# Kernel tuning notes

Measured on AMD Instinct MI355X. Metric: run time of the kernel, lower is better.

## Reference

```python
import jax, jax.numpy as jnp
import numpy as np

N = 16384      # batch (samples / graph nodes)
H = 256        # hid_dim
PRED_LEN = 24


def setup_inputs() -> dict:
    key = jax.random.key(0)
    ks = jax.random.split(key, 9)
    s = 1.0 / np.sqrt(H)  # PyTorch default init bound for GRUCell / Linear(H, 1)
    return {
        "encoder_out": jax.random.normal(ks[0], (N, H), dtype=jnp.float32),
        # input_proj = Linear(1, H): weight [H,1] flattened to [H], bound 1/sqrt(1)=1
        "w_proj": jax.random.uniform(ks[1], (H,), jnp.float32, -1.0, 1.0),
        "b_proj": jax.random.uniform(ks[2], (H,), jnp.float32, -1.0, 1.0),
        # GRUCell weights: [3H, H] ordered (reset, update, new) as in PyTorch
        "W_ih": jax.random.uniform(ks[3], (3 * H, H), jnp.float32, -s, s),
        "b_ih": jax.random.uniform(ks[4], (3 * H,), jnp.float32, -s, s),
        "W_hh": jax.random.uniform(ks[5], (3 * H, H), jnp.float32, -s, s),
        "b_hh": jax.random.uniform(ks[6], (3 * H,), jnp.float32, -s, s),
        # output_layer = Linear(H, 1): weight [1,H] flattened to [H]
        "w_out": jax.random.uniform(ks[7], (H,), jnp.float32, -s, s),
        "b_out": jax.random.uniform(ks[8], (1,), jnp.float32, -s, s),
    }


def reference(encoder_out, w_proj, b_proj, W_ih, b_ih, W_hh, b_hh, w_out, b_out):
    def step(carry, _):
        h, x = carry                       # h: [N,H], x: [N,1] scalar step input
        px = x * w_proj + b_proj           # input_proj(Linear(1,H)) -> [N,H]
        gi = px @ W_ih.T + b_ih            # [N,3H]
        gh = h @ W_hh.T + b_hh             # [N,3H]
        i_r, i_z, i_n = jnp.split(gi, 3, axis=1)
        h_r, h_z, h_n = jnp.split(gh, 3, axis=1)
        r = jax.nn.sigmoid(i_r + h_r)
        z = jax.nn.sigmoid(i_z + h_z)
        n = jnp.tanh(i_n + r * h_n)
        h_new = (1.0 - z) * n + z * h      # PyTorch GRUCell update
        pred = (h_new @ w_out)[:, None] + b_out  # output_layer -> [N,1]
        next_x = jax.lax.stop_gradient(pred)     # matches pred_t.detach()
        return (h_new, next_x), pred[:, 0]

    x0 = jnp.zeros((encoder_out.shape[0], 1), dtype=encoder_out.dtype)  # start token
    _, preds = jax.lax.scan(step, (encoder_out, x0), None, length=PRED_LEN)
    return preds.T  # [N, pred_len]
```

## Files before the change

### kernel.cpp

```cpp
#include <hip/hip_runtime.h>
#include <hip/hip_bf16.h>

#define NS 16384
#define H 256
#define TH 768
#define PRED 24
#define LDA 272
#define WS_NEEDED (425984)

typedef short bf16x8 __attribute__((ext_vector_type(8)));
typedef float floatx4 __attribute__((ext_vector_type(4)));

__device__ __forceinline__ float b2f(unsigned short u) {
    return __uint_as_float(((unsigned int)u) << 16);
}
__device__ __forceinline__ unsigned short f2b(float f) {
    unsigned int u = __float_as_uint(f);
    return (unsigned short)((u + 0x7FFFu + ((u >> 16) & 1u)) >> 16);
}
__device__ __forceinline__ float fsig(float v) {
    return __builtin_amdgcn_rcpf(1.0f + __expf(-v));
}
__device__ __forceinline__ float ftanh(float v) {
    return 1.0f - 2.0f * __builtin_amdgcn_rcpf(1.0f + __expf(2.0f * v));
}

__global__ void prep_proj(const void* __restrict__ WihP, const void* __restrict__ wprojP,
                          const void* __restrict__ bprojP, const void* __restrict__ bihP,
                          const void* __restrict__ bhhP, const void* __restrict__ woutP,
                          const void* __restrict__ boutP,
                          float* __restrict__ u, float* __restrict__ c,
                          float* __restrict__ bhn, float* __restrict__ wo,
                          float* __restrict__ b0) {
    const int j = blockIdx.x;
    const int lane = threadIdx.x;
    unsigned long long bm = __ballot(!(fabsf(b2f(((const unsigned short*)WihP)[lane])) <= 0.25f));
    const bool f32in = (bm != 0ull);

    float su = 0.f, sc = 0.f;
    if (f32in) {
        const float* row = (const float*)WihP + (size_t)j * H;
        const float* wp = (const float*)wprojP;
        const float* bp = (const float*)bprojP;
        for (int k = lane; k < H; k += 64) {
            float w = row[k];
            su = fmaf(w, wp[k], su); sc = fmaf(w, bp[k], sc);
        }
    } else {
        const unsigned short* row = (const unsigned short*)WihP + (size_t)j * H;
        const unsigned short* wp = (const unsigned short*)wprojP;
        const unsigned short* bp = (const unsigned short*)bprojP;
        for (int k = lane; k < H; k += 64) {
            float w = b2f(row[k]);
            su = fmaf(w, b2f(wp[k]), su); sc = fmaf(w, b2f(bp[k]), sc);
        }
    }
    for (int m = 32; m; m >>= 1) { su += __shfl_xor(su, m, 64); sc += __shfl_xor(sc, m, 64); }

    if (lane == 0) {
        float bih = f32in ? ((const float*)bihP)[j] : b2f(((const unsigned short*)bihP)[j]);
        float bhh = f32in ? ((const float*)bhhP)[j] : b2f(((const unsigned short*)bhhP)[j]);
        u[j] = su;
        c[j] = sc + bih + (j < 512 ? bhh : 0.f);
        if (j >= 512) bhn[j - 512] = bhh;
    }
    if (j < H && lane == 1)
        wo[j] = f32in ? ((const float*)woutP)[j] : b2f(((const unsigned short*)woutP)[j]);
    if (j == 0 && lane == 2)
        b0[0] = f32in ? ((const float*)boutP)[0] : b2f(((const unsigned short*)boutP)[0]);
}

__global__ void prep_swz2(const void* __restrict__ WhhP, unsigned short* __restrict__ Wp) {
    const int cidx = blockIdx.x * 256 + threadIdx.x;
    unsigned long long bm = __ballot(!(fabsf(b2f(((const unsigned short*)WhhP)[threadIdx.x & 63])) <= 0.25f));
    const bool f32in = (bm != 0ull);

    const int lane = cidx & 63;
    const int fi   = cidx >> 6;
    const int s    = fi & 1;
    const int g    = (fi >> 1) % 3;
    const int kk   = ((fi >> 1) / 3) & 7;
    const int w    = (fi >> 1) / 24;
    const size_t src = (size_t)(g * 256 + s * 128 + w * 16 + (lane & 15)) * H
                     + kk * 32 + (lane >> 4) * 8;
    unsigned short* dst = Wp + (size_t)cidx * 8;
    if (f32in) {
        const float* sp = (const float*)WhhP + src;
#pragma unroll
        for (int e = 0; e < 8; ++e) dst[e] = f2b(sp[e]);
    } else {
        const unsigned short* sp = (const unsigned short*)WhhP + src;
#pragma unroll
        for (int e = 0; e < 8; ++e) dst[e] = sp[e];
    }
}

__global__ __launch_bounds__(512, 2)
void decode_wres(const void* __restrict__ encP, const void* __restrict__ WihP,
                 const unsigned short* __restrict__ Wp,
                 const float* __restrict__ u, const float* __restrict__ c,
                 const float* __restrict__ bhnA, const float* __restrict__ woA,
                 const float* __restrict__ b0A, void* __restrict__ outP) {
    __shared__ __align__(16) unsigned short As[32 * LDA];
    __shared__ __align__(16) unsigned short Wl[8][6144];
    __shared__ float pred_part[8][32];
    __shared__ float pred_fin[32];
    __shared__ float pred_out[32][PRED];
    __shared__ int sflag;

    const int tid  = threadIdx.x;
    const int w    = tid >> 6;
    const int lane = tid & 63;
    const int lo   = lane & 15;
    const int quad = lane >> 4;
    const int m0   = blockIdx.x * 32;

    if (tid == 0) sflag = 0;
    __syncthreads();
    if (!(fabsf(b2f(((const unsigned short*)WihP)[tid])) <= 0.25f)) sflag = 1;
    __syncthreads();
    const bool f32in = (sflag != 0);

    const float*          encF = (const float*)encP;
    const unsigned short* encB = (const unsigned short*)encP;

    for (int i = tid; i < 32 * H; i += 512) {
        int r = i >> 8, col = i & 255;
        float hv = f32in ? encF[(size_t)(m0 + r) * H + col] : b2f(encB[(size_t)(m0 + r) * H + col]);
        As[r * LDA + col] = f2b(hv);
    }
    if (tid < 32) pred_fin[tid] = 0.f;

    float ur[2], uz[2], un[2], cr[2], cz[2], cn[2], bh[2], wov[2];
#pragma unroll
    for (int s = 0; s < 2; ++s) {
        const int jj = s * 128 + w * 16 + lo;
        ur[s] = u[jj];       uz[s] = u[256 + jj];       un[s] = u[512 + jj];
        cr[s] = c[jj];       cz[s] = c[256 + jj];       cn[s] = c[512 + jj];
        bh[s] = bhnA[jj];    wov[s] = woA[jj];
    }
    const float b0 = b0A[0];

    const unsigned short* wp = Wp + (size_t)w * 24576 + lane * 8;
    bf16x8 bW[6][3][2];
#pragma unroll
    for (int kk = 0; kk < 6; ++kk)
#pragma unroll
        for (int g = 0; g < 3; ++g)
#pragma unroll
            for (int s = 0; s < 2; ++s)
                bW[kk][g][s] = *(const bf16x8*)(wp + (size_t)((kk * 3 + g) * 2 + s) * 512);
#pragma unroll
    for (int kk = 6; kk < 8; ++kk)
#pragma unroll
        for (int g = 0; g < 3; ++g)
#pragma unroll
            for (int s = 0; s < 2; ++s) {
                bf16x8 v = *(const bf16x8*)(wp + (size_t)((kk * 3 + g) * 2 + s) * 512);
                *(bf16x8*)&Wl[w][(((kk - 6) * 3 + g) * 2 + s) * 512 + lane * 8] = v;
            }
    __syncthreads();

#pragma unroll 1
    for (int t = 0; t < PRED; ++t) {
        floatx4 acc[3][2][2];
#pragma unroll
        for (int g = 0; g < 3; ++g)
#pragma unroll
            for (int s = 0; s < 2; ++s)
#pragma unroll
                for (int im = 0; im < 2; ++im) acc[g][s][im] = (floatx4){0.f, 0.f, 0.f, 0.f};

#pragma unroll
        for (int kk = 0; kk < 8; ++kk) {
            bf16x8 a[2];
#pragma unroll
            for (int im = 0; im < 2; ++im)
                a[im] = *(const bf16x8*)&As[(im * 16 + lo) * LDA + kk * 32 + quad * 8];
            if (kk < 6) {
#pragma unroll
                for (int g = 0; g < 3; ++g)
#pragma unroll
                    for (int s = 0; s < 2; ++s)
#pragma unroll
                        for (int im = 0; im < 2; ++im)
                            acc[g][s][im] = __builtin_amdgcn_mfma_f32_16x16x32_bf16(
                                a[im], bW[kk][g][s], acc[g][s][im], 0, 0, 0);
            } else {
                bf16x8 b[3][2];
#pragma unroll
                for (int g = 0; g < 3; ++g)
#pragma unroll
                    for (int s = 0; s < 2; ++s)
                        b[g][s] = *(const bf16x8*)&Wl[w][(((kk - 6) * 3 + g) * 2 + s) * 512 + lane * 8];
#pragma unroll
                for (int g = 0; g < 3; ++g)
#pragma unroll
                    for (int s = 0; s < 2; ++s)
#pragma unroll
                        for (int im = 0; im < 2; ++im)
                            acc[g][s][im] = __builtin_amdgcn_mfma_f32_16x16x32_bf16(
                                a[im], b[g][s], acc[g][s][im], 0, 0, 0);
            }
        }
        __syncthreads();

#pragma unroll
        for (int im = 0; im < 2; ++im) {
#pragma unroll
            for (int v = 0; v < 4; ++v) {
                const int row = im * 16 + quad * 4 + v;
                const float xv = pred_fin[row];
                float pv = 0.f;
#pragma unroll
                for (int s = 0; s < 2; ++s) {
                    const int jj = s * 128 + w * 16 + lo;
                    const int hofs = row * LDA + jj;
                    const float hold = b2f(As[hofs]);
                    float r  = fsig(fmaf(xv, ur[s], cr[s]) + acc[0][s][im][v]);
                    float z  = fsig(fmaf(xv, uz[s], cz[s]) + acc[1][s][im][v]);
                    float n  = ftanh(fmaf(xv, un[s], cn[s]) + r * (acc[2][s][im][v] + bh[s]));
                    float hn = fmaf(z, hold - n, n);
                    As[hofs] = f2b(hn);
                    pv = fmaf(hn, wov[s], pv);
                }
                pv += __shfl_xor(pv, 1, 64);
                pv += __shfl_xor(pv, 2, 64);
                pv += __shfl_xor(pv, 4, 64);
                pv += __shfl_xor(pv, 8, 64);
                if (lo == 0) pred_part[w][row] = pv;
            }
        }
        __syncthreads();

        if (tid < 32) {
            float pr = b0;
#pragma unroll
            for (int ww = 0; ww < 8; ++ww) pr += pred_part[ww][tid];
            pred_fin[tid] = pr;
            pred_out[tid][t] = pr;
        }
    }
    __syncthreads();

    for (int i = tid; i < 32 * PRED; i += 512) {
        int row = i / PRED, tt = i % PRED;
        float pr = pred_out[row][tt];
        if (f32in) ((float*)outP)[(size_t)(m0 + row) * PRED + tt] = pr;
        else ((unsigned short*)outP)[(size_t)(m0 + row) * PRED + tt] = f2b(pr);
    }
}

__global__ __launch_bounds__(512, 2)
void decode_all(const void* __restrict__ encP,   const void* __restrict__ wprojP,
                const void* __restrict__ bprojP, const void* __restrict__ WihP,
                const void* __restrict__ bihP,   const void* __restrict__ WhhP,
                const void* __restrict__ bhhP,   const void* __restrict__ woutP,
                const void* __restrict__ boutP,  void* __restrict__ outP) {
    __shared__ __align__(16) unsigned short Asf[64 * LDA];
    __shared__ float u_lds[TH], c_lds[TH];
    __shared__ float bhn_lds[H], wo_lds[H];
    __shared__ float wp_lds[H], bp_lds[H];
    __shared__ float pred_lds[2][64];
    __shared__ int sflag;

    const int tid  = threadIdx.x;
    const int wid  = tid >> 6;
    const int lane = tid & 63;
    const int lo   = lane & 15;
    const int quad = lane >> 4;
    const int rh   = wid & 3;
    const int ch   = wid >> 2;
    const int m0   = blockIdx.x * 64;

    if (tid == 0) sflag = 0;
    __syncthreads();
    if (!(fabsf(b2f(((const unsigned short*)WihP)[tid])) <= 0.25f)) sflag = 1;
    __syncthreads();
    const bool f32in = (sflag != 0);

    const float*          encF = (const float*)encP;
    const unsigned short* encB = (const unsigned short*)encP;
    const unsigned short* WhhB = (const unsigned short*)WhhP;
    const float*          WhhF = (const float*)WhhP;

    if (tid < H) {
        wp_lds[tid] = f32in ? ((const float*)wprojP)[tid] : b2f(((const unsigned short*)wprojP)[tid]);
        bp_lds[tid] = f32in ? ((const float*)bprojP)[tid] : b2f(((const unsigned short*)bprojP)[tid]);
        wo_lds[tid] = f32in ? ((const float*)woutP)[tid]  : b2f(((const unsigned short*)woutP)[tid]);
    }
    __syncthreads();

    for (int j = tid; j < TH; j += 512) {
        float su = 0.f, sc = 0.f;
        if (f32in) {
            const float* row = (const float*)WihP + (size_t)j * H;
            for (int k = 0; k < H; ++k) { float w = row[k]; su = fmaf(w, wp_lds[k], su); sc = fmaf(w, bp_lds[k], sc); }
        } else {
            const unsigned short* row = (const unsigned short*)WihP + (size_t)j * H;
            for (int k = 0; k < H; ++k) { float w = b2f(row[k]); su = fmaf(w, wp_lds[k], su); sc = fmaf(w, bp_lds[k], sc); }
        }
        float bih = f32in ? ((const float*)bihP)[j] : b2f(((const unsigned short*)bihP)[j]);
        float bhh = f32in ? ((const float*)bhhP)[j] : b2f(((const unsigned short*)bhhP)[j]);
        u_lds[j] = su;
        c_lds[j] = sc + bih + (j < 512 ? bhh : 0.f);
        if (j >= 512) bhn_lds[j - 512] = bhh;
    }

    for (int i = tid; i < 64 * H; i += 512) {
        int r = i >> 8, col = i & 255;
        float hv = f32in ? encF[(size_t)(m0 + r) * H + col] : b2f(encB[(size_t)(m0 + r) * H + col]);
        Asf[r * LDA + col] = f2b(hv);
    }
    float hold[8][4];
#pragma unroll
    for (int s = 0; s < 8; ++s)
#pragma unroll
        for (int v = 0; v < 4; ++v) {
            int row = m0 + rh * 16 + quad * 4 + v;
            int jj  = ch * 128 + s * 16 + lo;
            hold[s][v] = f32in ? encF[(size_t)row * H + jj] : b2f(encB[(size_t)row * H + jj]);
        }
    const float b0 = f32in ? ((const float*)boutP)[0] : b2f(((const unsigned short*)boutP)[0]);

    float xm[4] = {0.f, 0.f, 0.f, 0.f};
    __syncthreads();

    const int aBase = (rh * 16 + lo) * LDA;
    const int wCol0 = ch * 128 + lo;

#pragma unroll 1
    for (int t = 0; t < PRED; ++t) {
        floatx4 acc[3][8];
#pragma unroll
        for (int g = 0; g < 3; ++g)
#pragma unroll
            for (int s = 0; s < 8; ++s) acc[g][s] = (floatx4){0.f, 0.f, 0.f, 0.f};

        if (f32in) {
#pragma unroll 1
            for (int kk = 0; kk < 8; ++kk) {
                bf16x8 a = *(const bf16x8*)&Asf[aBase + kk * 32 + quad * 8];
#pragma unroll
                for (int g = 0; g < 3; ++g)
#pragma unroll
                    for (int s = 0; s < 8; ++s) {
                        const float* wr = WhhF + (size_t)(g * 256 + wCol0 + s * 16) * H + kk * 32 + quad * 8;
                        float4 w0 = *(const float4*)wr;
                        float4 w1 = *(const float4*)(wr + 4);
                        bf16x8 b;
                        b[0] = (short)f2b(w0.x); b[1] = (short)f2b(w0.y);
                        b[2] = (short)f2b(w0.z); b[3] = (short)f2b(w0.w);
                        b[4] = (short)f2b(w1.x); b[5] = (short)f2b(w1.y);
                        b[6] = (short)f2b(w1.z); b[7] = (short)f2b(w1.w);
                        acc[g][s] = __builtin_amdgcn_mfma_f32_16x16x32_bf16(a, b, acc[g][s], 0, 0, 0);
                    }
            }
        } else {
#pragma unroll 1
            for (int kk = 0; kk < 8; ++kk) {
                bf16x8 a = *(const bf16x8*)&Asf[aBase + kk * 32 + quad * 8];
#pragma unroll
                for (int g = 0; g < 3; ++g)
#pragma unroll
                    for (int s = 0; s < 8; ++s) {
                        bf16x8 b = *(const bf16x8*)(WhhB + (size_t)(g * 256 + wCol0 + s * 16) * H + kk * 32 + quad * 8);
                        acc[g][s] = __builtin_amdgcn_mfma_f32_16x16x32_bf16(a, b, acc[g][s], 0, 0, 0);
                    }
            }
        }
        __syncthreads();

        float pp[4] = {0.f, 0.f, 0.f, 0.f};
#pragma unroll
        for (int s = 0; s < 8; ++s) {
            const int jj = ch * 128 + s * 16 + lo;
            const float urr = u_lds[jj], uzz = u_lds[256 + jj], unn = u_lds[512 + jj];
            const float crr = c_lds[jj], czz = c_lds[256 + jj], cnn = c_lds[512 + jj];
            const float bhn = bhn_lds[jj], wovv = wo_lds[jj];
#pragma unroll
            for (int v = 0; v < 4; ++v) {
                const float xv = xm[v];
                float r  = fsig(fmaf(xv, urr, crr) + acc[0][s][v]);
                float z  = fsig(fmaf(xv, uzz, czz) + acc[1][s][v]);
                float n  = ftanh(fmaf(xv, unn, cnn) + r * (acc[2][s][v] + bhn));
                float hn = fmaf(z, hold[s][v] - n, n);
                hold[s][v] = hn;
                Asf[(rh * 16 + quad * 4 + v) * LDA + jj] = f2b(hn);
                pp[v] = fmaf(hn, wovv, pp[v]);
            }
        }
#pragma unroll
        for (int v = 0; v < 4; ++v) {
            float pv = pp[v];
            pv += __shfl_xor(pv, 1, 64);
            pv += __shfl_xor(pv, 2, 64);
            pv += __shfl_xor(pv, 4, 64);
            pv += __shfl_xor(pv, 8, 64);
            if (lo == 0) pred_lds[ch][rh * 16 + quad * 4 + v] = pv;
        }
        __syncthreads();

#pragma unroll
        for (int v = 0; v < 4; ++v) {
            const int ml = rh * 16 + quad * 4 + v;
            xm[v] = b0 + pred_lds[0][ml] + pred_lds[1][ml];
        }
        if (tid < 64) {
            float pr = b0 + pred_lds[0][tid] + pred_lds[1][tid];
            if (f32in) ((float*)outP)[(size_t)(m0 + tid) * PRED + t] = pr;
            else ((unsigned short*)outP)[(size_t)(m0 + tid) * PRED + t] = f2b(pr);
        }
    }
}

extern "C" void kernel_launch(void* const* d_in, const int* in_sizes, int n_in,
                              void* d_out, int out_size, void* d_ws, size_t ws_size,
                              hipStream_t stream) {
    if (ws_size >= (size_t)WS_NEEDED) {
        char* ws = (char*)d_ws;
        unsigned short* Wp = (unsigned short*)ws;
        float* u   = (float*)(ws + 393216);
        float* c   = (float*)(ws + 396288);
        float* bhn = (float*)(ws + 399360);
        float* wo  = (float*)(ws + 400384);
        float* b0  = (float*)(ws + 401408);
        prep_proj<<<TH, 64, 0, stream>>>(d_in[3], d_in[1], d_in[2], d_in[4], d_in[6],
                                         d_in[7], d_in[8], u, c, bhn, wo, b0);
        prep_swz2<<<96, 256, 0, stream>>>(d_in[5], Wp);
        decode_wres<<<NS / 32, 512, 0, stream>>>(d_in[0], d_in[3], Wp, u, c, bhn, wo, b0, d_out);
    } else {
        decode_all<<<NS / 64, 512, 0, stream>>>(d_in[0], d_in[1], d_in[2], d_in[3],
                                                d_in[4], d_in[5], d_in[6], d_in[7],
                                                d_in[8], d_out);
    }
}
```

Baseline: 310.3 us.

## Fold output projection into MFMA and double-buffer hidden state to drop barriers

Each wave now computes the output-layer dot product for the previous hidden state redundantly with an extra MFMA against a zero-padded w_out B-operand, instead of a cross-wave reduction through shared memory. The hidden state is double-buffered in LDS so the per-step read/write hazard barrier can be removed, leaving one __syncthreads per step instead of three. This trades two extra MFMAs per k-step and doubled LDS for As against fewer barriers and less shuffle and reduction work. A final tail MFMA pass computes the last prediction, and the bf16 w_out weights add rounding to the fed-back input.

Result: slower. 319.9 us (+3.1%).

```diff
diff --git a/kernel.cpp b/kernel.cpp
--- a/kernel.cpp
+++ b/kernel.cpp
@@ -95,16 +95,25 @@
     }
 }
 
+__global__ void prep_wof(const float* __restrict__ wo, unsigned short* __restrict__ wf) {
+    const int idx = blockIdx.x * 256 + threadIdx.x;
+    const int kk   = idx >> 9;
+    const int lane = (idx >> 3) & 63;
+    const int e    = idx & 7;
+    unsigned short v = 0;
+    if ((lane & 15) == 0) v = f2b(wo[kk * 32 + (lane >> 4) * 8 + e]);
+    wf[idx] = v;
+}
+
 __global__ __launch_bounds__(512, 2)
-void decode_wres(const void* __restrict__ encP, const void* __restrict__ WihP,
-                 const unsigned short* __restrict__ Wp,
-                 const float* __restrict__ u, const float* __restrict__ c,
-                 const float* __restrict__ bhnA, const float* __restrict__ woA,
-                 const float* __restrict__ b0A, void* __restrict__ outP) {
-    __shared__ __align__(16) unsigned short As[32 * LDA];
+void decode_wr2(const void* __restrict__ encP, const void* __restrict__ WihP,
+                const unsigned short* __restrict__ Wp, const unsigned short* __restrict__ wf,
+                const float* __restrict__ u, const float* __restrict__ c,
+                const float* __restrict__ bhnA, const float* __restrict__ b0A,
+                void* __restrict__ outP) {
+    __shared__ __align__(16) unsigned short As[2][32 * LDA];
     __shared__ __align__(16) unsigned short Wl[8][6144];
-    __shared__ float pred_part[8][32];
-    __shared__ float pred_fin[32];
+    __shared__ __align__(16) unsigned short Wf[8 * 512];
     __shared__ float pred_out[32][PRED];
     __shared__ int sflag;
 
@@ -127,17 +136,17 @@
     for (int i = tid; i < 32 * H; i += 512) {
         int r = i >> 8, col = i & 255;
         float hv = f32in ? encF[(size_t)(m0 + r) * H + col] : b2f(encB[(size_t)(m0 + r) * H + col]);
-        As[r * LDA + col] = f2b(hv);
-    }
-    if (tid < 32) pred_fin[tid] = 0.f;
-
-    float ur[2], uz[2], un[2], cr[2], cz[2], cn[2], bh[2], wov[2];
+        As[0][r * LDA + col] = f2b(hv);
+    }
+    for (int i = tid; i < 4096; i += 512) Wf[i] = wf[i];
+
+    float ur[2], uz[2], un[2], cr[2], cz[2], cn[2], bh[2];
 #pragma unroll
     for (int s = 0; s < 2; ++s) {
         const int jj = s * 128 + w * 16 + lo;
         ur[s] = u[jj];       uz[s] = u[256 + jj];       un[s] = u[512 + jj];
         cr[s] = c[jj];       cz[s] = c[256 + jj];       cn[s] = c[512 + jj];
-        bh[s] = bhnA[jj];    wov[s] = woA[jj];
+        bh[s] = bhnA[jj];
     }
     const float b0 = b0A[0];
 
@@ -161,22 +170,30 @@
             }
     __syncthreads();
 
+    int p = 0;
 #pragma unroll 1
     for (int t = 0; t < PRED; ++t) {
         floatx4 acc[3][2][2];
+        floatx4 woacc[2];
 #pragma unroll
         for (int g = 0; g < 3; ++g)
 #pragma unroll
             for (int s = 0; s < 2; ++s)
 #pragma unroll
                 for (int im = 0; im < 2; ++im) acc[g][s][im] = (floatx4){0.f, 0.f, 0.f, 0.f};
+        woacc[0] = (floatx4){0.f, 0.f, 0.f, 0.f};
+        woacc[1] = (floatx4){0.f, 0.f, 0.f, 0.f};
+
+        const unsigned short* Ap = As[p];
+        unsigned short*       An = As[p ^ 1];
 
 #pragma unroll
         for (int kk = 0; kk < 8; ++kk) {
             bf16x8 a[2];
 #pragma unroll
             for (int im = 0; im < 2; ++im)
-                a[im] = *(const bf16x8*)&As[(im * 16 + lo) * LDA + kk * 32 + quad * 8];
+                a[im] = *(const bf16x8*)&Ap[(im * 16 + lo) * LDA + kk * 32 + quad * 8];
+            bf16x8 bwv = *(const bf16x8*)&Wf[kk * 512 + lane * 8];
             if (kk < 6) {
 #pragma unroll
                 for (int g = 0; g < 3; ++g)
@@ -202,43 +219,56 @@
                             acc[g][s][im] = __builtin_amdgcn_mfma_f32_16x16x32_bf16(
                                 a[im], b[g][s], acc[g][s][im], 0, 0, 0);
             }
-        }
-        __syncthreads();
+#pragma unroll
+            for (int im = 0; im < 2; ++im)
+                woacc[im] = __builtin_amdgcn_mfma_f32_16x16x32_bf16(a[im], bwv, woacc[im], 0, 0, 0);
+        }
 
 #pragma unroll
         for (int im = 0; im < 2; ++im) {
 #pragma unroll
             for (int v = 0; v < 4; ++v) {
                 const int row = im * 16 + quad * 4 + v;
-                const float xv = pred_fin[row];
-                float pv = 0.f;
+                float xv = 0.f;
+                if (t > 0) xv = b0 + __shfl(woacc[im][v], quad << 4, 64);
 #pragma unroll
                 for (int s = 0; s < 2; ++s) {
                     const int jj = s * 128 + w * 16 + lo;
                     const int hofs = row * LDA + jj;
-                    const float hold = b2f(As[hofs]);
+                    const float hold = b2f(Ap[hofs]);
                     float r  = fsig(fmaf(xv, ur[s], cr[s]) + acc[0][s][im][v]);
                     float z  = fsig(fmaf(xv, uz[s], cz[s]) + acc[1][s][im][v]);
                     float n  = ftanh(fmaf(xv, un[s], cn[s]) + r * (acc[2][s][im][v] + bh[s]));
                     float hn = fmaf(z, hold - n, n);
-                    As[hofs] = f2b(hn);
-                    pv = fmaf(hn, wov[s], pv);
+                    An[hofs] = f2b(hn);
                 }
-                pv += __shfl_xor(pv, 1, 64);
-                pv += __shfl_xor(pv, 2, 64);
-                pv += __shfl_xor(pv, 4, 64);
-                pv += __shfl_xor(pv, 8, 64);
-                if (lo == 0) pred_part[w][row] = pv;
+                if (w == 0 && lo == 0 && t > 0) pred_out[row][t - 1] = xv;
             }
         }
         __syncthreads();
-
-        if (tid < 32) {
-            float pr = b0;
-#pragma unroll
-            for (int ww = 0; ww < 8; ++ww) pr += pred_part[ww][tid];
-            pred_fin[tid] = pr;
-            pred_out[tid][t] = pr;
+        p ^= 1;
+    }
+
+    if (w == 0) {
+        const unsigned short* Ap = As[p];
+        floatx4 wa[2];
+        wa[0] = (floatx4){0.f, 0.f, 0.f, 0.f};
+        wa[1] = (floatx4){0.f, 0.f, 0.f, 0.f};
+#pragma unroll
+        for (int kk = 0; kk < 8; ++kk) {
+            bf16x8 bwv = *(const bf16x8*)&Wf[kk * 512 + lane * 8];
+#pragma unroll
+            for (int im = 0; im < 2; ++im) {
+                bf16x8 a = *(const bf16x8*)&Ap[(im * 16 + lo) * LDA + kk * 32 + quad * 8];
+                wa[im] = __builtin_amdgcn_mfma_f32_16x16x32_bf16(a, bwv, wa[im], 0, 0, 0);
+            }
+        }
+        if (lo == 0) {
+#pragma unroll
+            for (int im = 0; im < 2; ++im)
+#pragma unroll
+                for (int v = 0; v < 4; ++v)
+                    pred_out[im * 16 + quad * 4 + v][PRED - 1] = b0 + wa[im][v];
         }
     }
     __syncthreads();
@@ -425,10 +455,12 @@
         float* bhn = (float*)(ws + 399360);
         float* wo  = (float*)(ws + 400384);
         float* b0  = (float*)(ws + 401408);
+        unsigned short* wf = (unsigned short*)(ws + 402432);
         prep_proj<<<TH, 64, 0, stream>>>(d_in[3], d_in[1], d_in[2], d_in[4], d_in[6],
                                          d_in[7], d_in[8], u, c, bhn, wo, b0);
         prep_swz2<<<96, 256, 0, stream>>>(d_in[5], Wp);
-        decode_wres<<<NS / 32, 512, 0, stream>>>(d_in[0], d_in[3], Wp, u, c, bhn, wo, b0, d_out);
+        prep_wof<<<16, 256, 0, stream>>>(wo, wf);
+        decode_wr2<<<NS / 32, 512, 0, stream>>>(d_in[0], d_in[3], Wp, wf, u, c, bhn, b0, d_out);
     } else {
         decode_all<<<NS / 64, 512, 0, stream>>>(d_in[0], d_in[1], d_in[2], d_in[3],
                                                 d_in[4], d_in[5], d_in[6], d_in[7],
```

## Software-pipeline GRU decode by splitting rows into two half-tiles

Applied to the files above, without the earlier changes.

Splits the 32-row tile into two 16-row halves and interleaves them, so the MFMA K-loop of one half overlaps with the gate epilogue of the other. It also cuts barriers to two per step and splits the pred reduction across halves. Accumulator register pressure per half drops, but the schedule becomes more intricate, and correctness depends on pred_fin for each half being ready before its epilogue runs.

Result: faster. 296.1 us (-4.6%).

```diff
diff --git a/kernel.cpp b/kernel.cpp
--- a/kernel.cpp
+++ b/kernel.cpp
@@ -96,7 +96,7 @@
 }
 
 __global__ __launch_bounds__(512, 2)
-void decode_wres(const void* __restrict__ encP, const void* __restrict__ WihP,
+void decode_pipe(const void* __restrict__ encP, const void* __restrict__ WihP,
                  const unsigned short* __restrict__ Wp,
                  const float* __restrict__ u, const float* __restrict__ c,
                  const float* __restrict__ bhnA, const float* __restrict__ woA,
@@ -161,85 +161,95 @@
             }
     __syncthreads();
 
+#define KLOOP(ACC, IM)                                                                    \
+    do {                                                                                  \
+        _Pragma("unroll")                                                                 \
+        for (int g = 0; g < 3; ++g)                                                       \
+            _Pragma("unroll")                                                             \
+            for (int s = 0; s < 2; ++s) ACC[g][s] = (floatx4){0.f, 0.f, 0.f, 0.f};        \
+        _Pragma("unroll")                                                                 \
+        for (int kk = 0; kk < 8; ++kk) {                                                  \
+            bf16x8 a = *(const bf16x8*)&As[((IM) * 16 + lo) * LDA + kk * 32 + quad * 8];  \
+            if (kk < 6) {                                                                 \
+                _Pragma("unroll")                                                         \
+                for (int g = 0; g < 3; ++g)                                               \
+                    _Pragma("unroll")                                                     \
+                    for (int s = 0; s < 2; ++s)                                           \
+                        ACC[g][s] = __builtin_amdgcn_mfma_f32_16x16x32_bf16(              \
+                            a, bW[kk][g][s], ACC[g][s], 0, 0, 0);                         \
+            } else {                                                                      \
+                _Pragma("unroll")                                                         \
+                for (int g = 0; g < 3; ++g)                                               \
+                    _Pragma("unroll")                                                     \
+                    for (int s = 0; s < 2; ++s) {                                         \
+                        bf16x8 b = *(const bf16x8*)&Wl[w][(((kk - 6) * 3 + g) * 2 + s) * 512 + lane * 8]; \
+                        ACC[g][s] = __builtin_amdgcn_mfma_f32_16x16x32_bf16(              \
+                            a, b, ACC[g][s], 0, 0, 0);                                    \
+                    }                                                                     \
+            }                                                                             \
+        }                                                                                 \
+    } while (0)
+
+#define EPILOG(ACC, IM)                                                                   \
+    do {                                                                                  \
+        _Pragma("unroll")                                                                 \
+        for (int v = 0; v < 4; ++v) {                                                     \
+            const int row = (IM) * 16 + quad * 4 + v;                                     \
+            const float xv = pred_fin[row];                                               \
+            float pv = 0.f;                                                               \
+            _Pragma("unroll")                                                             \
+            for (int s = 0; s < 2; ++s) {                                                 \
+                const int jj = s * 128 + w * 16 + lo;                                     \
+                const int hofs = row * LDA + jj;                                          \
+                const float hold = b2f(As[hofs]);                                         \
+                float r  = fsig(fmaf(xv, ur[s], cr[s]) + ACC[0][s][v]);                   \
+                float z  = fsig(fmaf(xv, uz[s], cz[s]) + ACC[1][s][v]);                   \
+                float n  = ftanh(fmaf(xv, un[s], cn[s]) + r * (ACC[2][s][v] + bh[s]));    \
+                float hn = fmaf(z, hold - n, n);                                          \
+                As[hofs] = f2b(hn);                                                       \
+                pv = fmaf(hn, wov[s], pv);                                                \
+            }                                                                             \
+            pv += __shfl_xor(pv, 1, 64);                                                  \
+            pv += __shfl_xor(pv, 2, 64);                                                  \
+            pv += __shfl_xor(pv, 4, 64);                                                  \
+            pv += __shfl_xor(pv, 8, 64);                                                  \
+            if (lo == 0) pred_part[w][row] = pv;                                          \
+        }                                                                                 \
+    } while (0)
+
+    floatx4 accA[3][2], accB[3][2];
+    KLOOP(accA, 0);
+
 #pragma unroll 1
     for (int t = 0; t < PRED; ++t) {
-        floatx4 acc[3][2][2];
-#pragma unroll
-        for (int g = 0; g < 3; ++g)
-#pragma unroll
-            for (int s = 0; s < 2; ++s)
-#pragma unroll
-                for (int im = 0; im < 2; ++im) acc[g][s][im] = (floatx4){0.f, 0.f, 0.f, 0.f};
-
-#pragma unroll
-        for (int kk = 0; kk < 8; ++kk) {
-            bf16x8 a[2];
-#pragma unroll
-            for (int im = 0; im < 2; ++im)
-                a[im] = *(const bf16x8*)&As[(im * 16 + lo) * LDA + kk * 32 + quad * 8];
-            if (kk < 6) {
-#pragma unroll
-                for (int g = 0; g < 3; ++g)
-#pragma unroll
-                    for (int s = 0; s < 2; ++s)
-#pragma unroll
-                        for (int im = 0; im < 2; ++im)
-                            acc[g][s][im] = __builtin_amdgcn_mfma_f32_16x16x32_bf16(
-                                a[im], bW[kk][g][s], acc[g][s][im], 0, 0, 0);
-            } else {
-                bf16x8 b[3][2];
-#pragma unroll
-                for (int g = 0; g < 3; ++g)
-#pragma unroll
-                    for (int s = 0; s < 2; ++s)
-                        b[g][s] = *(const bf16x8*)&Wl[w][(((kk - 6) * 3 + g) * 2 + s) * 512 + lane * 8];
-#pragma unroll
-                for (int g = 0; g < 3; ++g)
-#pragma unroll
-                    for (int s = 0; s < 2; ++s)
-#pragma unroll
-                        for (int im = 0; im < 2; ++im)
-                            acc[g][s][im] = __builtin_amdgcn_mfma_f32_16x16x32_bf16(
-                                a[im], b[g][s], acc[g][s][im], 0, 0, 0);
-            }
-        }
+        if (t > 0 && tid >= 16 && tid < 32) {
+            float pr = b0;
+#pragma unroll
+            for (int ww = 0; ww < 8; ++ww) pr += pred_part[ww][tid];
+            pred_fin[tid] = pr;
+            pred_out[tid][t - 1] = pr;
+        }
+        EPILOG(accA, 0);
+        KLOOP(accB, 1);
         __syncthreads();
 
-#pragma unroll
-        for (int im = 0; im < 2; ++im) {
-#pragma unroll
-            for (int v = 0; v < 4; ++v) {
-                const int row = im * 16 + quad * 4 + v;
-                const float xv = pred_fin[row];
-                float pv = 0.f;
-#pragma unroll
-                for (int s = 0; s < 2; ++s) {
-                    const int jj = s * 128 + w * 16 + lo;
-                    const int hofs = row * LDA + jj;
-                    const float hold = b2f(As[hofs]);
-                    float r  = fsig(fmaf(xv, ur[s], cr[s]) + acc[0][s][im][v]);
-                    float z  = fsig(fmaf(xv, uz[s], cz[s]) + acc[1][s][im][v]);
-                    float n  = ftanh(fmaf(xv, un[s], cn[s]) + r * (acc[2][s][im][v] + bh[s]));
-                    float hn = fmaf(z, hold - n, n);
-                    As[hofs] = f2b(hn);
-                    pv = fmaf(hn, wov[s], pv);
-                }
-                pv += __shfl_xor(pv, 1, 64);
-                pv += __shfl_xor(pv, 2, 64);
-                pv += __shfl_xor(pv, 4, 64);
-                pv += __shfl_xor(pv, 8, 64);
-                if (lo == 0) pred_part[w][row] = pv;
-            }
-        }
-        __syncthreads();
-
-        if (tid < 32) {
+        if (tid < 16) {
             float pr = b0;
 #pragma unroll
             for (int ww = 0; ww < 8; ++ww) pr += pred_part[ww][tid];
             pred_fin[tid] = pr;
             pred_out[tid][t] = pr;
         }
+        EPILOG(accB, 1);
+        if (t < PRED - 1) KLOOP(accA, 0);
+        __syncthreads();
+    }
+
+    if (tid >= 16 && tid < 32) {
+        float pr = b0;
+#pragma unroll
+        for (int ww = 0; ww < 8; ++ww) pr += pred_part[ww][tid];
+        pred_out[tid][PRED - 1] = pr;
     }
     __syncthreads();
 
@@ -249,6 +259,8 @@
         if (f32in) ((float*)outP)[(size_t)(m0 + row) * PRED + tt] = pr;
         else ((unsigned short*)outP)[(size_t)(m0 + row) * PRED + tt] = f2b(pr);
     }
+#undef KLOOP
+#undef EPILOG
 }
 
 __global__ __launch_bounds__(512, 2)
@@ -428,7 +440,7 @@
         prep_proj<<<TH, 64, 0, stream>>>(d_in[3], d_in[1], d_in[2], d_in[4], d_in[6],
                                          d_in[7], d_in[8], u, c, bhn, wo, b0);
         prep_swz2<<<96, 256, 0, stream>>>(d_in[5], Wp);
-        decode_wres<<<NS / 32, 512, 0, stream>>>(d_in[0], d_in[3], Wp, u, c, bhn, wo, b0, d_out);
+        decode_pipe<<<NS / 32, 512, 0, stream>>>(d_in[0], d_in[3], Wp, u, c, bhn, wo, b0, d_out);
     } else {
         decode_all<<<NS / 64, 512, 0, stream>>>(d_in[0], d_in[1], d_in[2], d_in[3],
                                                 d_in[4], d_in[5], d_in[6], d_in[7],
```
